# Kernel optimization log

Hardware: AMD Instinct MI355X
Metric: run time of the kernel (lower is better)

Reference implementation:

```python
import jax, jax.numpy as jnp
import numpy as np

B, C_IN, H, W = 8, 64, 256, 256
C_OUT, K, GROUPS, REP_DIM = 64, 3, 64, 512


def setup_inputs() -> dict:
    key = jax.random.key(0)
    k1, k2, k3 = jax.random.split(key, 3)
    x = jax.random.normal(k1, (B, C_IN, H, W), dtype=jnp.float32)
    representation = jax.random.normal(k2, (B, REP_DIM), dtype=jnp.float32)
    # Linear(representation_dim -> out_channels*k*k, bias=False) weight, [out_features, in_features]
    w_key = jax.random.normal(k3, (C_OUT * K * K, REP_DIM), dtype=jnp.float32) * (REP_DIM ** -0.5)
    return {"x": x, "representation": representation, "w_key": w_key}


def reference(x, representation, w_key):
    b = x.shape[0]
    fpg = C_IN // GROUPS          # features_per_group (input channels per group)
    opg = C_OUT // GROUPS         # output channels per group
    pad = K // 2

    # compress_key: Linear (no bias) + LeakyReLU(0.1)
    # per-sample dynamic kernels: [b, out_channels, k, k] (the repeat_interleave in the
    # original just copies this single spatial kernel across all fpg in-channels of a group)
    kern = jax.nn.leaky_relu(representation @ w_key.T, negative_slope=0.1)
    kern = kern.reshape(b, GROUPS, opg, K, K)

    # reflection pad (matches torch ReflectionPad2d)
    xp = jnp.pad(x, ((0, 0), (0, 0), (pad, pad), (pad, pad)), mode='reflect')

    # since each output channel's kernel is identical across its group's in-channels,
    # conv(sum of group channels) == sum of convs: pre-sum in-channels per group
    xg = xp.reshape(b, GROUPS, fpg, H + 2 * pad, W + 2 * pad).sum(axis=2)  # [b,g,hp,wp]

    # accumulate over the K*K kernel taps (small fixed loop), fully vectorized over b,g,h,w
    out = jnp.zeros((b, GROUPS, opg, H, W), dtype=x.dtype)
    for dy in range(K):
        for dx in range(K):
            out = out + jnp.einsum('bghw,bgo->bgohw',
                                   xg[:, :, dy:dy + H, dx:dx + W],
                                   kern[:, :, :, dy, dx])
    return out.reshape(b, C_OUT, H, W)
```

## Files before the change

kernel.cpp:

```cpp
#include <hip/hip_runtime.h>

#define B_  8
#define C_  64
#define H_  256
#define W_  256
#define REP_ 512

__global__ __launch_bounds__(256) void compute_kern_k(const float* __restrict__ rep,
                                                      const float* __restrict__ wkey,
                                                      float* __restrict__ kern) {
    int wave = blockIdx.x * 4 + (threadIdx.x >> 6);
    int lane = threadIdx.x & 63;
    int b = wave / 576;
    int o = wave - b * 576;
    const float* wrow = wkey + (size_t)o * REP_;
    const float* rrow = rep  + (size_t)b * REP_;
    float acc = 0.f;
#pragma unroll
    for (int i = 0; i < REP_ / 64; ++i) {
        int r = lane + i * 64;
        acc += rrow[r] * wrow[r];
    }
#pragma unroll
    for (int off = 32; off > 0; off >>= 1)
        acc += __shfl_xor(acc, off, 64);
    if (lane == 0) {
        float v = acc;
        kern[wave] = v > 0.f ? v : 0.1f * v;
    }
}

__global__ __launch_bounds__(256) void dwconv3x3_strip8(const float* __restrict__ x,
                                                        const float* __restrict__ kern,
                                                        float* __restrict__ out) {
    int plane = blockIdx.x >> 3;
    int strip = blockIdx.x & 7;
    int wv   = threadIdx.x >> 6;
    int lane = threadIdx.x & 63;
    int r0 = strip * 32 + wv * 8;
    int c4 = lane << 2;

    const float* pin  = x   + (size_t)plane * (H_ * W_);
    float*       pout = out + (size_t)plane * (H_ * W_);
    const float* kp   = kern + plane * 9;
    float k[9];
#pragma unroll
    for (int i = 0; i < 9; ++i) k[i] = kp[i];

    float4 raw[10];
#pragma unroll
    for (int i = 0; i < 10; ++i) {
        int t = r0 - 1 + i;
        int rr = (t < 0) ? -t : ((t >= H_) ? (2 * H_ - 2 - t) : t);
        raw[i] = *(const float4*)(pin + rr * W_ + c4);
    }

    float lft[10], rgt[10];
#pragma unroll
    for (int i = 0; i < 10; ++i) {
        float lv = __shfl(raw[i].w, lane - 1, 64);
        lft[i] = (lane == 0) ? raw[i].y : lv;
        float rv = __shfl(raw[i].x, lane + 1, 64);
        rgt[i] = (lane == 63) ? raw[i].z : rv;
    }

    auto e = [&](int i, int t) -> float {
        if (t == 0) return lft[i];
        if (t == 5) return rgt[i];
        return ((const float*)&raw[i])[t - 1];
    };

#pragma unroll
    for (int j = 0; j < 8; ++j) {
        float4 o4;
        float* op = (float*)&o4;
#pragma unroll
        for (int t = 0; t < 4; ++t) {
            op[t] = k[0] * e(j, t)     + k[1] * e(j, t + 1)     + k[2] * e(j, t + 2)
                  + k[3] * e(j + 1, t) + k[4] * e(j + 1, t + 1) + k[5] * e(j + 1, t + 2)
                  + k[6] * e(j + 2, t) + k[7] * e(j + 2, t + 1) + k[8] * e(j + 2, t + 2);
        }
        *(float4*)(pout + (size_t)(r0 + j) * W_ + c4) = o4;
    }
}

extern "C" void kernel_launch(void* const* d_in, const int* in_sizes, int n_in,
                              void* d_out, int out_size, void* d_ws, size_t ws_size,
                              hipStream_t stream) {
    const float* x    = (const float*)d_in[0];
    const float* rep  = (const float*)d_in[1];
    const float* wkey = (const float*)d_in[2];
    float* out  = (float*)d_out;
    float* kern = (float*)d_ws;

    compute_kern_k<<<1152, 256, 0, stream>>>(rep, wkey, kern);
    dwconv3x3_strip8<<<4096, 256, 0, stream>>>(x, kern, out);
}
```

Measured before the change: 238.8 us.

## Pipeline row loads through a register ring and use nontemporal stores

```diff
diff --git a/kernel.cpp b/kernel.cpp
--- a/kernel.cpp
+++ b/kernel.cpp
@@ -1,4 +1,6 @@
 #include <hip/hip_runtime.h>
+
+typedef float f32x4 __attribute__((ext_vector_type(4)));
 
 #define B_  8
 #define C_  64
@@ -30,14 +32,17 @@
     }
 }
 
-__global__ __launch_bounds__(256) void dwconv3x3_strip8(const float* __restrict__ x,
-                                                        const float* __restrict__ kern,
-                                                        float* __restrict__ out) {
-    int plane = blockIdx.x >> 3;
-    int strip = blockIdx.x & 7;
+#define RING 6
+#define RPW  16
+
+__global__ __launch_bounds__(256) void dwconv3x3_pipe(const float* __restrict__ x,
+                                                      const float* __restrict__ kern,
+                                                      float* __restrict__ out) {
+    int plane   = blockIdx.x >> 2;
+    int quarter = blockIdx.x & 3;
     int wv   = threadIdx.x >> 6;
     int lane = threadIdx.x & 63;
-    int r0 = strip * 32 + wv * 8;
+    int r0 = quarter * 64 + wv * RPW;
     int c4 = lane << 2;
 
     const float* pin  = x   + (size_t)plane * (H_ * W_);
@@ -47,40 +52,45 @@
 #pragma unroll
     for (int i = 0; i < 9; ++i) k[i] = kp[i];
 
-    float4 raw[10];
-#pragma unroll
-    for (int i = 0; i < 10; ++i) {
+    f32x4 raw[RING];
+    float lft[RING], rgt[RING];
+
+    auto issue = [&](int i) {
         int t = r0 - 1 + i;
         int rr = (t < 0) ? -t : ((t >= H_) ? (2 * H_ - 2 - t) : t);
-        raw[i] = *(const float4*)(pin + rr * W_ + c4);
-    }
-
-    float lft[10], rgt[10];
-#pragma unroll
-    for (int i = 0; i < 10; ++i) {
-        float lv = __shfl(raw[i].w, lane - 1, 64);
-        lft[i] = (lane == 0) ? raw[i].y : lv;
-        float rv = __shfl(raw[i].x, lane + 1, 64);
-        rgt[i] = (lane == 63) ? raw[i].z : rv;
-    }
-
+        raw[i % RING] = *(const f32x4*)(pin + (size_t)rr * W_ + c4);
+    };
+    auto prep = [&](int i) {
+        int s = i % RING;
+        float lv = __shfl(raw[s][3], lane - 1, 64);
+        lft[s] = (lane == 0) ? raw[s][1] : lv;
+        float rv = __shfl(raw[s][0], lane + 1, 64);
+        rgt[s] = (lane == 63) ? raw[s][2] : rv;
+    };
     auto e = [&](int i, int t) -> float {
-        if (t == 0) return lft[i];
-        if (t == 5) return rgt[i];
-        return ((const float*)&raw[i])[t - 1];
+        int s = i % RING;
+        if (t == 0) return lft[s];
+        if (t == 5) return rgt[s];
+        return raw[s][t - 1];
     };
 
 #pragma unroll
-    for (int j = 0; j < 8; ++j) {
-        float4 o4;
-        float* op = (float*)&o4;
+    for (int i = 0; i < RING; ++i) issue(i);
+    prep(0);
+    prep(1);
+
+#pragma unroll
+    for (int j = 0; j < RPW; ++j) {
+        prep(j + 2);
+        f32x4 o4;
 #pragma unroll
         for (int t = 0; t < 4; ++t) {
-            op[t] = k[0] * e(j, t)     + k[1] * e(j, t + 1)     + k[2] * e(j, t + 2)
+            o4[t] = k[0] * e(j, t)     + k[1] * e(j, t + 1)     + k[2] * e(j, t + 2)
                   + k[3] * e(j + 1, t) + k[4] * e(j + 1, t + 1) + k[5] * e(j + 1, t + 2)
                   + k[6] * e(j + 2, t) + k[7] * e(j + 2, t + 1) + k[8] * e(j + 2, t + 2);
         }
-        *(float4*)(pout + (size_t)(r0 + j) * W_ + c4) = o4;
+        __builtin_nontemporal_store(o4, (f32x4*)(pout + (size_t)(r0 + j) * W_ + c4));
+        if (j + RING < RPW + 2) issue(j + RING);
     }
 }
 
@@ -94,5 +104,5 @@
     float* kern = (float*)d_ws;
 
     compute_kern_k<<<1152, 256, 0, stream>>>(rep, wkey, kern);
-    dwconv3x3_strip8<<<4096, 256, 0, stream>>>(x, kern, out);
+    dwconv3x3_pipe<<<2048, 256, 0, stream>>>(x, kern, out);
 }
```

Result: no change. 238.0 us (-0.3%).
